# Kernel optimization log

Measured on AMD Instinct MI355X. Metric: run time of the kernel, lower is better.

## Reference

```python
import jax, jax.numpy as jnp
import numpy as np

S = 8          # num_syndromes (distance-3 surface code)
Q = 9          # num_qubits
F = 64         # n_node_features
H = 256        # hidden_size
ITERS = 3      # n_iters
B = 65536      # batch_size (shots)
N = B * S      # total nodes in batched graph
E = 2097152    # num edges (~avg degree 4)


def setup_inputs() -> dict:
    key = jax.random.key(0)
    ks = jax.random.split(key, 20)
    sc = 0.05
    inp = {
        "syndromes": jax.random.uniform(ks[0], (N, 1), dtype=jnp.float32),
        "edge_index": jax.random.randint(ks[1], (2, E), 0, N, dtype=jnp.int64),
        "batch_size": B,
        # embed: Linear(1, F)
        "embed_W": jax.random.normal(ks[2], (1, F), jnp.float32) * sc,
        "embed_b": jnp.zeros((F,), jnp.float32),
        # GCNConv per iter: weight (F,F) + bias (F,)
        "gcn_W": jax.random.normal(ks[3], (ITERS, F, F), jnp.float32) * sc,
        "gcn_b": jnp.zeros((ITERS, F), jnp.float32),
        # refine MLP per iter: F->H->F
        "ref_W1": jax.random.normal(ks[4], (ITERS, F, H), jnp.float32) * sc,
        "ref_b1": jnp.zeros((ITERS, H), jnp.float32),
        "ref_W2": jax.random.normal(ks[5], (ITERS, H, F), jnp.float32) * sc,
        "ref_b2": jnp.zeros((ITERS, F), jnp.float32),
        # error head per iter: F*S -> H -> H//2 -> Q
        "head_W1": jax.random.normal(ks[6], (ITERS, F * S, H), jnp.float32) * sc,
        "head_b1": jnp.zeros((ITERS, H), jnp.float32),
        "head_W2": jax.random.normal(ks[7], (ITERS, H, H // 2), jnp.float32) * sc,
        "head_b2": jnp.zeros((ITERS, H // 2), jnp.float32),
        "head_W3": jax.random.normal(ks[8], (ITERS, H // 2, Q), jnp.float32) * sc,
        "head_b3": jnp.zeros((ITERS, Q), jnp.float32),
    }
    return inp


def _gcn(x, src, dst, norm, W, b, n_nodes):
    # x' = D^{-1/2} (A+I) D^{-1/2} (x W) + b   (PyG GCNConv, eval mode)
    xw = x @ W                                  # [N, F]
    msg = xw[src] * norm[:, None]               # gather + edge-normalize
    out = jax.ops.segment_sum(msg, dst, num_segments=n_nodes)
    return out + b


def reference(syndromes, edge_index, batch_size,
              embed_W, embed_b, gcn_W, gcn_b,
              ref_W1, ref_b1, ref_W2, ref_b2,
              head_W1, head_b1, head_W2, head_b2, head_W3, head_b3):
    n_nodes = syndromes.shape[0]
    loops = jnp.arange(n_nodes, dtype=edge_index.dtype)
    src = jnp.concatenate([edge_index[0], loops])
    dst = jnp.concatenate([edge_index[1], loops])
    deg = jnp.zeros((n_nodes,), syndromes.dtype).at[dst].add(1.0)
    dinv = 1.0 / jnp.sqrt(deg)                  # deg >= 1 due to self-loops
    norm = dinv[src] * dinv[dst]

    h = syndromes @ embed_W + embed_b           # [N, F]
    outs = []
    for i in range(ITERS):
        h = _gcn(h, src, dst, norm, gcn_W[i], gcn_b[i], n_nodes)
        h = jax.nn.relu(h)
        r = jax.nn.relu(h @ ref_W1[i] + ref_b1[i]) @ ref_W2[i] + ref_b2[i]
        h = jax.nn.relu(h + r)
        h_all = h.reshape(batch_size, -1)        # [B, S*F]
        z = jax.nn.relu(h_all @ head_W1[i] + head_b1[i])
        z = jax.nn.relu(z @ head_W2[i] + head_b2[i])
        outs.append(jax.nn.sigmoid(z @ head_W3[i] + head_b3[i]))  # [B, Q]
    return tuple(outs)
```

## Files before the change

kernel.cpp:

```cpp
#include <hip/hip_runtime.h>
#include <cstdint>

#define NN 524288
#define NB 65536
#define NQ 9
#define NEDGE 2097152
#define NITERS 3
#define NBUCK 256
#define BCAP 16384

typedef __attribute__((ext_vector_type(8))) short bf16x8;
typedef __attribute__((ext_vector_type(4))) float f32x4;

__device__ __forceinline__ unsigned short f2b(float f) {
    union { float f; unsigned u; } v; v.f = f;
    unsigned u = v.u;
    u += 0x7FFFu + ((u >> 16) & 1u);
    return (unsigned short)(u >> 16);
}
__device__ __forceinline__ float b2f(unsigned short b) {
    union { unsigned u; float f; } v; v.u = ((unsigned)b) << 16;
    return v.f;
}
__device__ __forceinline__ float frelu(float v) { return v > 0.f ? v : 0.f; }

__device__ __forceinline__ int sw64(int r, int c)  { return r * 64  + (c ^ ((r & 7) << 3)); }
__device__ __forceinline__ int sw128(int r, int c) { return r * 128 + (c ^ ((r & 7) << 3)); }
__device__ __forceinline__ int sw256(int r, int c) { return r * 256 + (c ^ ((r & 7) << 3)); }


__global__ void k_zero256(int* __restrict__ gcount) {
    gcount[threadIdx.x] = 0;
}

__global__ __launch_bounds__(1024) void k_binA(const int* __restrict__ eidx,
                                               uint2* __restrict__ tmp,
                                               int* __restrict__ gcount) {
    __shared__ int acnt[NBUCK];
    __shared__ int abase[NBUCK];
    __shared__ uint2 ed[8192];
    const int t = threadIdx.x;
    if (t < NBUCK) acnt[t] = 0;
    __syncthreads();
    const int e0 = blockIdx.x * 8192;
#pragma unroll
    for (int r = 0; r < 8; ++r) {
        int e = e0 + r * 1024 + t;
        int s = eidx[e], d = eidx[NEDGE + e];
        ed[r * 1024 + t] = make_uint2((unsigned)s, (unsigned)d);
        atomicAdd(&acnt[d >> 11], 1);
    }
    __syncthreads();
    if (t < NBUCK) {
        abase[t] = atomicAdd(&gcount[t], acnt[t]);
        acnt[t] = 0;
    }
    __syncthreads();
#pragma unroll
    for (int r = 0; r < 8; ++r) {
        uint2 sd = ed[r * 1024 + t];
        int b = sd.y >> 11;
        int slot = abase[b] + atomicAdd(&acnt[b], 1);
        tmp[(size_t)b * BCAP + slot] = sd;
    }
}

__global__ void k_scanB(const int* __restrict__ gcount, int* __restrict__ bbase,
                        int* __restrict__ rowptr) {
    __shared__ int sd[NBUCK];
    int t = threadIdx.x;
    int v = gcount[t];
    sd[t] = v; __syncthreads();
    for (int o = 1; o < NBUCK; o <<= 1) {
        int u = (t >= o) ? sd[t - o] : 0;
        __syncthreads();
        sd[t] += u;
        __syncthreads();
    }
    bbase[t] = sd[t] - v;
    if (t == 0) rowptr[NN] = NEDGE;
}

__global__ __launch_bounds__(1024) void k_binB(const uint2* __restrict__ tmp,
                                               const int* __restrict__ gcount,
                                               const int* __restrict__ bbase,
                                               int* __restrict__ rowptr,
                                               float* __restrict__ dinv,
                                               int* __restrict__ srcs) {
    __shared__ int A[2048];
    __shared__ int B[2048];
    __shared__ int lcur[2048];
    const int t = threadIdx.x;
    const int b = blockIdx.x;
    const int nb = gcount[b];
    const int base = bbase[b];
    const uint2* te = tmp + (size_t)b * BCAP;

    A[t] = 0; A[t + 1024] = 0;
    __syncthreads();
    for (int i = t; i < nb; i += 1024)
        atomicAdd(&A[te[i].y & 2047], 1);
    __syncthreads();

    {
        int n0 = (b << 11) + t;
        dinv[n0] = rsqrtf(1.f + (float)A[t]);
        dinv[n0 + 1024] = rsqrtf(1.f + (float)A[t + 1024]);
    }

    int* src = A; int* dst = B;
    for (int o = 1; o < 2048; o <<= 1) {
        for (int j = t; j < 2048; j += 1024) {
            int v = src[j];
            if (j >= o) v += src[j - o];
            dst[j] = v;
        }
        __syncthreads();
        int* tp = src; src = dst; dst = tp;
    }
    for (int j = t; j < 2048; j += 1024) {
        int excl = (j == 0) ? 0 : src[j - 1];
        int gpos = base + excl;
        rowptr[(b << 11) + j] = gpos;
        lcur[j] = gpos;
    }
    __syncthreads();

    for (int i = t; i < nb; i += 1024) {
        uint2 sd = te[i];
        int pos = atomicAdd(&lcur[sd.y & 2047], 1);
        srcs[pos] = (int)sd.x;
    }
}

__global__ void k_trans_all(const float* __restrict__ gcnW, const float* __restrict__ rW1,
                            const float* __restrict__ rW2, const float* __restrict__ hW1,
                            const float* __restrict__ hW2, const float* __restrict__ hW3,
                            unsigned short* __restrict__ gcnWt, unsigned short* __restrict__ rW1t,
                            unsigned short* __restrict__ rW2t, unsigned short* __restrict__ hW1t,
                            unsigned short* __restrict__ hW2t, unsigned short* __restrict__ hW3t) {
    int o = blockIdx.x * 256 + threadIdx.x;
    const float* W; unsigned short* Wt; int K, M, base;
    if      (o < 12288)  { W = gcnW; Wt = gcnWt; K = 64;  M = 64;  base = 0; }
    else if (o < 61440)  { W = rW1;  Wt = rW1t;  K = 64;  M = 256; base = 12288; }
    else if (o < 110592) { W = rW2;  Wt = rW2t;  K = 256; M = 64;  base = 61440; }
    else if (o < 503808) { W = hW1;  Wt = hW1t;  K = 512; M = 256; base = 110592; }
    else if (o < 602112) { W = hW2;  Wt = hW2t;  K = 256; M = 128; base = 503808; }
    else if (o < 605568) { W = hW3;  Wt = hW3t;  K = 128; M = 9;   base = 602112; }
    else return;
    int rel = o - base;
    int km = K * M;
    int it = rel / km;
    int rem = rel - it * km;
    int m = rem / K;
    int k = rem - m * K;
    Wt[rel] = f2b(W[(size_t)it * km + (size_t)k * M + m]);
}



template<bool EMBED>
__global__ __launch_bounds__(256, 6) void k_gcnref(
    const int* __restrict__ rowptr, const int* __restrict__ srcs,
    const float* __restrict__ dinv,
    const float* __restrict__ syn, const float* __restrict__ embW,
    const float* __restrict__ embB,
    const unsigned short* __restrict__ hin,
    const unsigned short* __restrict__ Wgt, const float* __restrict__ bg,
    const unsigned short* __restrict__ W1t, const float* __restrict__ b1,
    const unsigned short* __restrict__ W2t, const float* __restrict__ b2,
    unsigned short* __restrict__ hout)
{
    __shared__ unsigned short tl[64 * 64];
    __shared__ unsigned short zl[64 * 64];
    const int tid = threadIdx.x, wid = tid >> 6, l = tid & 63;
    const int lr = l & 15, lkq = l >> 4;
    const int g = l >> 4, i = l & 15;
    const int rowBase = blockIdx.x * 64;
    const int nb = rowBase + wid * 16;

    float4 ew4, eb4;
    if (EMBED) {
        ew4 = *(const float4*)(embW + i * 4);
        eb4 = *(const float4*)(embB + i * 4);
    }

    for (int q = 0; q < 4; ++q) {
        const int node = nb + q * 4 + g;
        int beg = rowptr[node];
        int deg = rowptr[node + 1] - beg;
        int   sl = (i < deg) ? srcs[beg + i] : node;
        float wl = (i < deg) ? dinv[sl] : 0.f;

        float dn = dinv[node];
        float a0, a1, a2, a3;
        if (EMBED) {
            float s0 = syn[node];
            a0 = (s0 * ew4.x + eb4.x) * dn;
            a1 = (s0 * ew4.y + eb4.y) * dn;
            a2 = (s0 * ew4.z + eb4.z) * dn;
            a3 = (s0 * ew4.w + eb4.w) * dn;
        } else {
            ushort4 sv = *(const ushort4*)(hin + (size_t)node * 64 + i * 4);
            a0 = b2f(sv.x) * dn; a1 = b2f(sv.y) * dn;
            a2 = b2f(sv.z) * dn; a3 = b2f(sv.w) * dn;
        }

        int dmax = max(max(__shfl(deg, 0), __shfl(deg, 16)),
                       max(__shfl(deg, 32), __shfl(deg, 48)));
        int dfast = dmax < 16 ? dmax : 16;

        for (int p = 0; p < dfast; p += 8) {
            int   s[8]; float w[8];
#pragma unroll
            for (int u = 0; u < 8; ++u) {
                int idx = (l & 48) + p + u;
                s[u] = __shfl(sl, idx);
                w[u] = __shfl(wl, idx);
            }
            if (EMBED) {
                float sy[8];
#pragma unroll
                for (int u = 0; u < 8; ++u) sy[u] = syn[s[u]];
#pragma unroll
                for (int u = 0; u < 8; ++u) {
                    a0 += (sy[u] * ew4.x + eb4.x) * w[u];
                    a1 += (sy[u] * ew4.y + eb4.y) * w[u];
                    a2 += (sy[u] * ew4.z + eb4.z) * w[u];
                    a3 += (sy[u] * ew4.w + eb4.w) * w[u];
                }
            } else {
                ushort4 v[8];
#pragma unroll
                for (int u = 0; u < 8; ++u)
                    v[u] = *(const ushort4*)(hin + (size_t)s[u] * 64 + i * 4);
#pragma unroll
                for (int u = 0; u < 8; ++u) {
                    a0 += b2f(v[u].x) * w[u];
                    a1 += b2f(v[u].y) * w[u];
                    a2 += b2f(v[u].z) * w[u];
                    a3 += b2f(v[u].w) * w[u];
                }
            }
        }
        if (deg > 16) {
            for (int t = 16; t < deg; ++t) {
                int st = srcs[beg + t];
                float wt = dinv[st];
                if (EMBED) {
                    float sy = syn[st];
                    a0 += (sy * ew4.x + eb4.x) * wt;
                    a1 += (sy * ew4.y + eb4.y) * wt;
                    a2 += (sy * ew4.z + eb4.z) * wt;
                    a3 += (sy * ew4.w + eb4.w) * wt;
                } else {
                    ushort4 v = *(const ushort4*)(hin + (size_t)st * 64 + i * 4);
                    a0 += b2f(v.x) * wt; a1 += b2f(v.y) * wt;
                    a2 += b2f(v.z) * wt; a3 += b2f(v.w) * wt;
                }
            }
        }
        ushort4 o;
        o.x = f2b(a0 * dn); o.y = f2b(a1 * dn);
        o.z = f2b(a2 * dn); o.w = f2b(a3 * dn);
        *(ushort4*)&tl[sw64(wid * 16 + q * 4 + g, i * 4)] = o;
    }

    f32x4 ag[4];
#pragma unroll
    for (int mg = 0; mg < 4; ++mg) ag[mg] = (f32x4){0.f, 0.f, 0.f, 0.f};
#pragma unroll
    for (int kc = 0; kc < 64; kc += 32) {
        bf16x8 bfr = *(const bf16x8*)&tl[sw64(wid * 16 + lr, kc + lkq * 8)];
#pragma unroll
        for (int mg = 0; mg < 4; ++mg) {
            bf16x8 a = *(const bf16x8*)(Wgt + (size_t)(mg * 16 + lr) * 64 + kc + lkq * 8);
            ag[mg] = __builtin_amdgcn_mfma_f32_16x16x32_bf16(a, bfr, ag[mg], 0, 0, 0);
        }
    }
#pragma unroll
    for (int mg = 0; mg < 4; ++mg) {
        int m0 = mg * 16 + lkq * 4;
        float4 bb = *(const float4*)(bg + m0);
        ushort4 o;
        o.x = f2b(frelu(ag[mg][0] + bb.x));
        o.y = f2b(frelu(ag[mg][1] + bb.y));
        o.z = f2b(frelu(ag[mg][2] + bb.z));
        o.w = f2b(frelu(ag[mg][3] + bb.w));
        *(ushort4*)&tl[sw64(wid * 16 + lr, m0)] = o;
    }
    __syncthreads();

    f32x4 r2[4];
#pragma unroll
    for (int mg = 0; mg < 4; ++mg) r2[mg] = (f32x4){0.f, 0.f, 0.f, 0.f};

#pragma unroll
    for (int qt = 0; qt < 4; ++qt) {
        f32x4 z1a[4];
#pragma unroll
        for (int ng = 0; ng < 4; ++ng) z1a[ng] = (f32x4){0.f, 0.f, 0.f, 0.f};
#pragma unroll
        for (int kc = 0; kc < 64; kc += 32) {
            bf16x8 a = *(const bf16x8*)(W1t +
                (size_t)(qt * 64 + wid * 16 + lr) * 64 + kc + lkq * 8);
#pragma unroll
            for (int ng = 0; ng < 4; ++ng) {
                bf16x8 bfr = *(const bf16x8*)&tl[sw64(ng * 16 + lr, kc + lkq * 8)];
                z1a[ng] = __builtin_amdgcn_mfma_f32_16x16x32_bf16(a, bfr, z1a[ng], 0, 0, 0);
            }
        }
        {
            int m0 = wid * 16 + lkq * 4;
            float4 bb = *(const float4*)(b1 + qt * 64 + m0);
#pragma unroll
            for (int ng = 0; ng < 4; ++ng) {
                int n = ng * 16 + lr;
                ushort4 o;
                o.x = f2b(frelu(z1a[ng][0] + bb.x));
                o.y = f2b(frelu(z1a[ng][1] + bb.y));
                o.z = f2b(frelu(z1a[ng][2] + bb.z));
                o.w = f2b(frelu(z1a[ng][3] + bb.w));
                *(ushort4*)&zl[sw64(n, m0)] = o;
            }
        }
        __syncthreads();

#pragma unroll
        for (int kc = 0; kc < 64; kc += 32) {
            bf16x8 bz = *(const bf16x8*)&zl[sw64(wid * 16 + lr, kc + lkq * 8)];
#pragma unroll
            for (int mg = 0; mg < 4; ++mg) {
                bf16x8 a = *(const bf16x8*)(W2t +
                    (size_t)(mg * 16 + lr) * 256 + qt * 64 + kc + lkq * 8);
                r2[mg] = __builtin_amdgcn_mfma_f32_16x16x32_bf16(a, bz, r2[mg], 0, 0, 0);
            }
        }
        if (qt < 3) __syncthreads();
    }

    {
        int n = wid * 16 + lr;
#pragma unroll
        for (int mg = 0; mg < 4; ++mg) {
            int m0 = mg * 16 + lkq * 4;
            float4 bb = *(const float4*)(b2 + m0);
            ushort4 rs = *(const ushort4*)&tl[sw64(n, m0)];
            ushort4 o;
            o.x = f2b(frelu(r2[mg][0] + bb.x + b2f(rs.x)));
            o.y = f2b(frelu(r2[mg][1] + bb.y + b2f(rs.y)));
            o.z = f2b(frelu(r2[mg][2] + bb.z + b2f(rs.z)));
            o.w = f2b(frelu(r2[mg][3] + bb.w + b2f(rs.w)));
            *(ushort4*)&tl[sw64(n, m0)] = o;
        }
    }
    __syncthreads();
    {
        int r = tid >> 2, c16 = (tid & 3) * 16;
        bf16x8 v0 = *(const bf16x8*)&tl[sw64(r, c16)];
        bf16x8 v1 = *(const bf16x8*)&tl[sw64(r, c16 + 8)];
        *(bf16x8*)(hout + (size_t)(rowBase + r) * 64 + c16) = v0;
        *(bf16x8*)(hout + (size_t)(rowBase + r) * 64 + c16 + 8) = v1;
    }
}

__global__ __launch_bounds__(256, 4) void k_head(
    const unsigned short* __restrict__ hb,
    const unsigned short* __restrict__ W1t,
    const float* __restrict__ b1,
    const unsigned short* __restrict__ W2t,
    const float* __restrict__ b2,
    const unsigned short* __restrict__ W3t,
    const float* __restrict__ b3,
    float* __restrict__ out)
{
    __shared__ unsigned short sm[64 * 256];
    const int tid = threadIdx.x, wid = tid >> 6, l = tid & 63;
    const int lr = l & 15, lkq = l >> 4;
    const unsigned short* hall = hb + (size_t)blockIdx.x * 64 * 512;

    f32x4 acc1[4][4];
#pragma unroll
    for (int mg = 0; mg < 4; ++mg)
#pragma unroll
        for (int ng = 0; ng < 4; ++ng) acc1[mg][ng] = (f32x4){0.f, 0.f, 0.f, 0.f};

    for (int kc = 0; kc < 512; kc += 32) {
        bf16x8 bfr[4];
#pragma unroll
        for (int ng = 0; ng < 4; ++ng)
            bfr[ng] = *(const bf16x8*)(hall + (size_t)(ng * 16 + lr) * 512 + kc + lkq * 8);
#pragma unroll
        for (int mg = 0; mg < 4; ++mg) {
            bf16x8 a = *(const bf16x8*)(W1t + (size_t)(wid * 64 + mg * 16 + lr) * 512 + kc + lkq * 8);
#pragma unroll
            for (int ng = 0; ng < 4; ++ng)
                acc1[mg][ng] = __builtin_amdgcn_mfma_f32_16x16x32_bf16(a, bfr[ng], acc1[mg][ng], 0, 0, 0);
        }
    }
#pragma unroll
    for (int mg = 0; mg < 4; ++mg) {
        int m0 = wid * 64 + mg * 16 + lkq * 4;
        float4 bb = *(const float4*)(b1 + m0);
#pragma unroll
        for (int ng = 0; ng < 4; ++ng) {
            int n = ng * 16 + lr;
            ushort4 o;
            o.x = f2b(frelu(acc1[mg][ng][0] + bb.x));
            o.y = f2b(frelu(acc1[mg][ng][1] + bb.y));
            o.z = f2b(frelu(acc1[mg][ng][2] + bb.z));
            o.w = f2b(frelu(acc1[mg][ng][3] + bb.w));
            *(ushort4*)&sm[sw256(n, m0)] = o;
        }
    }
    __syncthreads();

    f32x4 acc2[2][4];
#pragma unroll
    for (int mg = 0; mg < 2; ++mg)
#pragma unroll
        for (int ng = 0; ng < 4; ++ng) acc2[mg][ng] = (f32x4){0.f, 0.f, 0.f, 0.f};
#pragma unroll
    for (int kc = 0; kc < 256; kc += 32) {
        bf16x8 bfr[4];
#pragma unroll
        for (int ng = 0; ng < 4; ++ng)
            bfr[ng] = *(const bf16x8*)&sm[sw256(ng * 16 + lr, kc + lkq * 8)];
#pragma unroll
        for (int mg = 0; mg < 2; ++mg) {
            bf16x8 a = *(const bf16x8*)(W2t + (size_t)(wid * 32 + mg * 16 + lr) * 256 + kc + lkq * 8);
#pragma unroll
            for (int ng = 0; ng < 4; ++ng)
                acc2[mg][ng] = __builtin_amdgcn_mfma_f32_16x16x32_bf16(a, bfr[ng], acc2[mg][ng], 0, 0, 0);
        }
    }
    __syncthreads();

#pragma unroll
    for (int mg = 0; mg < 2; ++mg) {
        int m0 = wid * 32 + mg * 16 + lkq * 4;
        float4 bb = *(const float4*)(b2 + m0);
#pragma unroll
        for (int ng = 0; ng < 4; ++ng) {
            int n = ng * 16 + lr;
            ushort4 o;
            o.x = f2b(frelu(acc2[mg][ng][0] + bb.x));
            o.y = f2b(frelu(acc2[mg][ng][1] + bb.y));
            o.z = f2b(frelu(acc2[mg][ng][2] + bb.z));
            o.w = f2b(frelu(acc2[mg][ng][3] + bb.w));
            *(ushort4*)&sm[sw128(n, m0)] = o;
        }
    }
    __syncthreads();

    f32x4 a3 = (f32x4){0.f, 0.f, 0.f, 0.f};
    int arow = lr < 9 ? lr : 8;
#pragma unroll
    for (int kc = 0; kc < 128; kc += 32) {
        bf16x8 bz = *(const bf16x8*)&sm[sw128(wid * 16 + lr, kc + lkq * 8)];
        bf16x8 a = *(const bf16x8*)(W3t + (size_t)arow * 128 + kc + lkq * 8);
        a3 = __builtin_amdgcn_mfma_f32_16x16x32_bf16(a, bz, a3, 0, 0, 0);
    }
    {
        long shot = (long)blockIdx.x * 64 + wid * 16 + lr;
#pragma unroll
        for (int r = 0; r < 4; ++r) {
            int m = lkq * 4 + r;
            if (m < 9) out[shot * 9 + m] = 1.f / (1.f + expf(-(a3[r] + b3[m])));
        }
    }
}


extern "C" void kernel_launch(void* const* d_in, const int* in_sizes, int n_in,
                              void* d_out, int out_size, void* d_ws, size_t ws_size,
                              hipStream_t stream) {
    const float* syn  = (const float*)d_in[0];
    const int*   eidx = (const int*)d_in[1];
    const float* embW = (const float*)d_in[3];
    const float* embB = (const float*)d_in[4];
    const float* gcnW = (const float*)d_in[5];
    const float* gcnB = (const float*)d_in[6];
    const float* rW1  = (const float*)d_in[7];
    const float* rB1  = (const float*)d_in[8];
    const float* rW2  = (const float*)d_in[9];
    const float* rB2  = (const float*)d_in[10];
    const float* hW1  = (const float*)d_in[11];
    const float* hB1  = (const float*)d_in[12];
    const float* hW2  = (const float*)d_in[13];
    const float* hB2  = (const float*)d_in[14];
    const float* hW3  = (const float*)d_in[15];
    const float* hB3  = (const float*)d_in[16];
    float* out = (float*)d_out;

    unsigned short* h0     = (unsigned short*)d_ws;
    unsigned short* h1     = h0 + (size_t)NN * 64;
    int*            srcs   = (int*)(h1 + (size_t)NN * 64);
    int*            rowptr = srcs + NEDGE;
    float*          dinv   = (float*)(rowptr + NN + 16);
    uint2*          tmp    = (uint2*)(dinv + NN);
    int*            gcount = (int*)(tmp + (size_t)NBUCK * BCAP);
    int*            bbase  = gcount + NBUCK;
    unsigned short* gcnWt  = (unsigned short*)(bbase + NBUCK + 16);
    unsigned short* rW1t   = gcnWt + 3 * 64 * 64;
    unsigned short* rW2t   = rW1t + 3 * 64 * 256;
    unsigned short* hW1t   = rW2t + 3 * 256 * 64;
    unsigned short* hW2t   = hW1t + 3 * 512 * 256;
    unsigned short* hW3t   = hW2t + 3 * 256 * 128;

    k_trans_all<<<(605568 + 255) / 256, 256, 0, stream>>>(
        gcnW, rW1, rW2, hW1, hW2, hW3, gcnWt, rW1t, rW2t, hW1t, hW2t, hW3t);
    k_zero256<<<1, NBUCK, 0, stream>>>(gcount);
    k_binA<<<NEDGE / 8192, 1024, 0, stream>>>(eidx, tmp, gcount);
    k_scanB<<<1, NBUCK, 0, stream>>>(gcount, bbase, rowptr);
    k_binB<<<NBUCK, 1024, 0, stream>>>(tmp, gcount, bbase, rowptr, dinv, srcs);

    unsigned short* hcur = h0;
    unsigned short* hnxt = h1;
    for (int i = 0; i < NITERS; ++i) {
        unsigned short* hdst = (i == 0) ? h0 : hnxt;
        if (i == 0) {
            k_gcnref<true><<<NN / 64, 256, 0, stream>>>(
                rowptr, srcs, dinv, syn, embW, embB, nullptr,
                gcnWt, gcnB,
                rW1t, rB1, rW2t, rB2, h0);
        } else {
            k_gcnref<false><<<NN / 64, 256, 0, stream>>>(
                rowptr, srcs, dinv, nullptr, nullptr, nullptr, hcur,
                gcnWt + (size_t)i * 64 * 64, gcnB + (size_t)i * 64,
                rW1t + (size_t)i * 64 * 256, rB1 + (size_t)i * 256,
                rW2t + (size_t)i * 256 * 64, rB2 + (size_t)i * 64, hdst);
        }
        k_head<<<NB / 64, 256, 0, stream>>>(
            hdst,
            hW1t + (size_t)i * 512 * 256, hB1 + (size_t)i * 256,
            hW2t + (size_t)i * 256 * 128, hB2 + (size_t)i * 128,
            hW3t + (size_t)i * 128 * 9,   hB3 + (size_t)i * 9,
            out + (size_t)i * NB * NQ);
        if (i == 0) { hcur = h0; hnxt = h1; }
        else { unsigned short* t = hcur; hcur = hdst; hnxt = t; }
    }
}
```

Baseline: 1.001 ms.

## Pre-scale node features by dinv and pack edge bins into single words

Node features are now stored pre-multiplied by D^{-1/2} (hs buffers) by the producing kernel. The gather loop then becomes a plain sum, with no per-neighbour dinv lookup or multiply and no separate embed path; a zero padding row replaces the masked weight. Edge binning packs source and local destination into one 32-bit word, halving the temp traffic, and that temp buffer now reuses the hsB space. The cost is an extra pre-scaled bf16 write per node per iteration, a new small embedding kernel, and an extra bf16 rounding of the scaled features.

```diff
diff --git a/kernel.cpp b/kernel.cpp
--- a/kernel.cpp
+++ b/kernel.cpp
@@ -34,7 +34,7 @@
 }
 
 __global__ __launch_bounds__(1024) void k_binA(const int* __restrict__ eidx,
-                                               uint2* __restrict__ tmp,
+                                               unsigned* __restrict__ tmp,
                                                int* __restrict__ gcount) {
     __shared__ int acnt[NBUCK];
     __shared__ int abase[NBUCK];
@@ -61,7 +61,7 @@
         uint2 sd = ed[r * 1024 + t];
         int b = sd.y >> 11;
         int slot = abase[b] + atomicAdd(&acnt[b], 1);
-        tmp[(size_t)b * BCAP + slot] = sd;
+        tmp[(size_t)b * BCAP + slot] = sd.x | ((sd.y & 2047u) << 19);
     }
 }
 
@@ -81,7 +81,7 @@
     if (t == 0) rowptr[NN] = NEDGE;
 }
 
-__global__ __launch_bounds__(1024) void k_binB(const uint2* __restrict__ tmp,
+__global__ __launch_bounds__(1024) void k_binB(const unsigned* __restrict__ tmp,
                                                const int* __restrict__ gcount,
                                                const int* __restrict__ bbase,
                                                int* __restrict__ rowptr,
@@ -94,12 +94,12 @@
     const int b = blockIdx.x;
     const int nb = gcount[b];
     const int base = bbase[b];
-    const uint2* te = tmp + (size_t)b * BCAP;
+    const unsigned* te = tmp + (size_t)b * BCAP;
 
     A[t] = 0; A[t + 1024] = 0;
     __syncthreads();
     for (int i = t; i < nb; i += 1024)
-        atomicAdd(&A[te[i].y & 2047], 1);
+        atomicAdd(&A[te[i] >> 19], 1);
     __syncthreads();
 
     {
@@ -127,10 +127,32 @@
     __syncthreads();
 
     for (int i = t; i < nb; i += 1024) {
-        uint2 sd = te[i];
-        int pos = atomicAdd(&lcur[sd.y & 2047], 1);
-        srcs[pos] = (int)sd.x;
-    }
+        unsigned v = te[i];
+        int pos = atomicAdd(&lcur[v >> 19], 1);
+        srcs[pos] = (int)(v & 0x7FFFFu);
+    }
+}
+
+__global__ void k_hs0(const float* __restrict__ syn, const float* __restrict__ dinv,
+                      const float* __restrict__ embW, const float* __restrict__ embB,
+                      unsigned short* __restrict__ hsA, unsigned short* __restrict__ hsB) {
+    int idx = blockIdx.x * 256 + threadIdx.x;
+    int n = idx >> 4, f4 = (idx & 15) * 4;
+    if (n > NN) return;
+    if (n == NN) {
+        *(ushort4*)(hsA + (size_t)NN * 64 + f4) = make_ushort4(0, 0, 0, 0);
+        *(ushort4*)(hsB + (size_t)NN * 64 + f4) = make_ushort4(0, 0, 0, 0);
+        return;
+    }
+    float s = syn[n], dn = dinv[n];
+    float4 ew = *(const float4*)(embW + f4);
+    float4 eb = *(const float4*)(embB + f4);
+    ushort4 o;
+    o.x = f2b(dn * (s * ew.x + eb.x));
+    o.y = f2b(dn * (s * ew.y + eb.y));
+    o.z = f2b(dn * (s * ew.z + eb.z));
+    o.w = f2b(dn * (s * ew.w + eb.w));
+    *(ushort4*)(hsA + (size_t)n * 64 + f4) = o;
 }
 
 __global__ void k_trans_all(const float* __restrict__ gcnW, const float* __restrict__ rW1,
@@ -159,17 +181,14 @@
 
 
 
-template<bool EMBED>
 __global__ __launch_bounds__(256, 6) void k_gcnref(
     const int* __restrict__ rowptr, const int* __restrict__ srcs,
     const float* __restrict__ dinv,
-    const float* __restrict__ syn, const float* __restrict__ embW,
-    const float* __restrict__ embB,
-    const unsigned short* __restrict__ hin,
+    const unsigned short* __restrict__ hsin,
     const unsigned short* __restrict__ Wgt, const float* __restrict__ bg,
     const unsigned short* __restrict__ W1t, const float* __restrict__ b1,
     const unsigned short* __restrict__ W2t, const float* __restrict__ b2,
-    unsigned short* __restrict__ hout)
+    unsigned short* __restrict__ hout, unsigned short* __restrict__ hsout)
 {
     __shared__ unsigned short tl[64 * 64];
     __shared__ unsigned short zl[64 * 64];
@@ -179,85 +198,40 @@
     const int rowBase = blockIdx.x * 64;
     const int nb = rowBase + wid * 16;
 
-    float4 ew4, eb4;
-    if (EMBED) {
-        ew4 = *(const float4*)(embW + i * 4);
-        eb4 = *(const float4*)(embB + i * 4);
-    }
-
     for (int q = 0; q < 4; ++q) {
         const int node = nb + q * 4 + g;
         int beg = rowptr[node];
         int deg = rowptr[node + 1] - beg;
-        int   sl = (i < deg) ? srcs[beg + i] : node;
-        float wl = (i < deg) ? dinv[sl] : 0.f;
+        int sl = (i < deg) ? srcs[beg + i] : NN;
 
         float dn = dinv[node];
-        float a0, a1, a2, a3;
-        if (EMBED) {
-            float s0 = syn[node];
-            a0 = (s0 * ew4.x + eb4.x) * dn;
-            a1 = (s0 * ew4.y + eb4.y) * dn;
-            a2 = (s0 * ew4.z + eb4.z) * dn;
-            a3 = (s0 * ew4.w + eb4.w) * dn;
-        } else {
-            ushort4 sv = *(const ushort4*)(hin + (size_t)node * 64 + i * 4);
-            a0 = b2f(sv.x) * dn; a1 = b2f(sv.y) * dn;
-            a2 = b2f(sv.z) * dn; a3 = b2f(sv.w) * dn;
-        }
+        ushort4 sv = *(const ushort4*)(hsin + (size_t)node * 64 + i * 4);
+        float a0 = b2f(sv.x), a1 = b2f(sv.y), a2 = b2f(sv.z), a3 = b2f(sv.w);
 
         int dmax = max(max(__shfl(deg, 0), __shfl(deg, 16)),
                        max(__shfl(deg, 32), __shfl(deg, 48)));
         int dfast = dmax < 16 ? dmax : 16;
 
         for (int p = 0; p < dfast; p += 8) {
-            int   s[8]; float w[8];
+            int s[8];
+#pragma unroll
+            for (int u = 0; u < 8; ++u)
+                s[u] = __shfl(sl, (l & 48) + p + u);
+            ushort4 v[8];
+#pragma unroll
+            for (int u = 0; u < 8; ++u)
+                v[u] = *(const ushort4*)(hsin + (size_t)s[u] * 64 + i * 4);
 #pragma unroll
             for (int u = 0; u < 8; ++u) {
-                int idx = (l & 48) + p + u;
-                s[u] = __shfl(sl, idx);
-                w[u] = __shfl(wl, idx);
-            }
-            if (EMBED) {
-                float sy[8];
-#pragma unroll
-                for (int u = 0; u < 8; ++u) sy[u] = syn[s[u]];
-#pragma unroll
-                for (int u = 0; u < 8; ++u) {
-                    a0 += (sy[u] * ew4.x + eb4.x) * w[u];
-                    a1 += (sy[u] * ew4.y + eb4.y) * w[u];
-                    a2 += (sy[u] * ew4.z + eb4.z) * w[u];
-                    a3 += (sy[u] * ew4.w + eb4.w) * w[u];
-                }
-            } else {
-                ushort4 v[8];
-#pragma unroll
-                for (int u = 0; u < 8; ++u)
-                    v[u] = *(const ushort4*)(hin + (size_t)s[u] * 64 + i * 4);
-#pragma unroll
-                for (int u = 0; u < 8; ++u) {
-                    a0 += b2f(v[u].x) * w[u];
-                    a1 += b2f(v[u].y) * w[u];
-                    a2 += b2f(v[u].z) * w[u];
-                    a3 += b2f(v[u].w) * w[u];
-                }
+                a0 += b2f(v[u].x); a1 += b2f(v[u].y);
+                a2 += b2f(v[u].z); a3 += b2f(v[u].w);
             }
         }
         if (deg > 16) {
             for (int t = 16; t < deg; ++t) {
                 int st = srcs[beg + t];
-                float wt = dinv[st];
-                if (EMBED) {
-                    float sy = syn[st];
-                    a0 += (sy * ew4.x + eb4.x) * wt;
-                    a1 += (sy * ew4.y + eb4.y) * wt;
-                    a2 += (sy * ew4.z + eb4.z) * wt;
-                    a3 += (sy * ew4.w + eb4.w) * wt;
-                } else {
-                    ushort4 v = *(const ushort4*)(hin + (size_t)st * 64 + i * 4);
-                    a0 += b2f(v.x) * wt; a1 += b2f(v.y) * wt;
-                    a2 += b2f(v.z) * wt; a3 += b2f(v.w) * wt;
-                }
+                ushort4 v = *(const ushort4*)(hsin + (size_t)st * 64 + i * 4);
+                a0 += b2f(v.x); a1 += b2f(v.y); a2 += b2f(v.z); a3 += b2f(v.w);
             }
         }
         ushort4 o;
@@ -361,6 +335,17 @@
         bf16x8 v1 = *(const bf16x8*)&tl[sw64(r, c16 + 8)];
         *(bf16x8*)(hout + (size_t)(rowBase + r) * 64 + c16) = v0;
         *(bf16x8*)(hout + (size_t)(rowBase + r) * 64 + c16 + 8) = v1;
+        if (hsout) {
+            float dv = dinv[rowBase + r];
+            bf16x8 w0, w1;
+#pragma unroll
+            for (int j = 0; j < 8; ++j) {
+                w0[j] = (short)f2b(b2f((unsigned short)v0[j]) * dv);
+                w1[j] = (short)f2b(b2f((unsigned short)v1[j]) * dv);
+            }
+            *(bf16x8*)(hsout + (size_t)(rowBase + r) * 64 + c16) = w0;
+            *(bf16x8*)(hsout + (size_t)(rowBase + r) * 64 + c16 + 8) = w1;
+        }
     }
 }
 
@@ -493,13 +478,13 @@
     const float* hB3  = (const float*)d_in[16];
     float* out = (float*)d_out;
 
-    unsigned short* h0     = (unsigned short*)d_ws;
-    unsigned short* h1     = h0 + (size_t)NN * 64;
-    int*            srcs   = (int*)(h1 + (size_t)NN * 64);
+    unsigned short* h      = (unsigned short*)d_ws;
+    unsigned short* hsA    = h + (size_t)NN * 64;
+    unsigned short* hsB    = hsA + (size_t)NN * 64 + 64;
+    int*            srcs   = (int*)(hsB + (size_t)NN * 64 + 64);
     int*            rowptr = srcs + NEDGE;
     float*          dinv   = (float*)(rowptr + NN + 16);
-    uint2*          tmp    = (uint2*)(dinv + NN);
-    int*            gcount = (int*)(tmp + (size_t)NBUCK * BCAP);
+    int*            gcount = (int*)(dinv + NN);
     int*            bbase  = gcount + NBUCK;
     unsigned short* gcnWt  = (unsigned short*)(bbase + NBUCK + 16);
     unsigned short* rW1t   = gcnWt + 3 * 64 * 64;
@@ -507,6 +492,7 @@
     unsigned short* hW1t   = rW2t + 3 * 256 * 64;
     unsigned short* hW2t   = hW1t + 3 * 512 * 256;
     unsigned short* hW3t   = hW2t + 3 * 256 * 128;
+    unsigned*       tmp    = (unsigned*)hsB;
 
     k_trans_all<<<(605568 + 255) / 256, 256, 0, stream>>>(
         gcnW, rW1, rW2, hW1, hW2, hW3, gcnWt, rW1t, rW2t, hW1t, hW2t, hW3t);
@@ -514,30 +500,22 @@
     k_binA<<<NEDGE / 8192, 1024, 0, stream>>>(eidx, tmp, gcount);
     k_scanB<<<1, NBUCK, 0, stream>>>(gcount, bbase, rowptr);
     k_binB<<<NBUCK, 1024, 0, stream>>>(tmp, gcount, bbase, rowptr, dinv, srcs);
-
-    unsigned short* hcur = h0;
-    unsigned short* hnxt = h1;
+    k_hs0<<<((NN + 1) * 16 + 255) / 256, 256, 0, stream>>>(syn, dinv, embW, embB, hsA, hsB);
+
     for (int i = 0; i < NITERS; ++i) {
-        unsigned short* hdst = (i == 0) ? h0 : hnxt;
-        if (i == 0) {
-            k_gcnref<true><<<NN / 64, 256, 0, stream>>>(
-                rowptr, srcs, dinv, syn, embW, embB, nullptr,
-                gcnWt, gcnB,
-                rW1t, rB1, rW2t, rB2, h0);
-        } else {
-            k_gcnref<false><<<NN / 64, 256, 0, stream>>>(
-                rowptr, srcs, dinv, nullptr, nullptr, nullptr, hcur,
-                gcnWt + (size_t)i * 64 * 64, gcnB + (size_t)i * 64,
-                rW1t + (size_t)i * 64 * 256, rB1 + (size_t)i * 256,
-                rW2t + (size_t)i * 256 * 64, rB2 + (size_t)i * 64, hdst);
-        }
+        unsigned short* hsin  = (i & 1) ? hsB : hsA;
+        unsigned short* hsout = (i == 2) ? nullptr : ((i & 1) ? hsA : hsB);
+        k_gcnref<<<NN / 64, 256, 0, stream>>>(
+            rowptr, srcs, dinv, hsin,
+            gcnWt + (size_t)i * 64 * 64, gcnB + (size_t)i * 64,
+            rW1t + (size_t)i * 64 * 256, rB1 + (size_t)i * 256,
+            rW2t + (size_t)i * 256 * 64, rB2 + (size_t)i * 64,
+            h, hsout);
         k_head<<<NB / 64, 256, 0, stream>>>(
-            hdst,
+            h,
             hW1t + (size_t)i * 512 * 256, hB1 + (size_t)i * 256,
             hW2t + (size_t)i * 256 * 128, hB2 + (size_t)i * 128,
             hW3t + (size_t)i * 128 * 9,   hB3 + (size_t)i * 9,
             out + (size_t)i * NB * NQ);
-        if (i == 0) { hcur = h0; hnxt = h1; }
-        else { unsigned short* t = hcur; hcur = hdst; hnxt = t; }
-    }
-}
+    }
+}
```

New measurement: 1.024 ms. +2.3%, slower.
